# Kernel optimization log

Measured on AMD Instinct MI355X. Metric: run time of the kernel, lower is better.

The kernel has to match this reference:

```python
import jax, jax.numpy as jnp
import numpy as np

B, T, E, H = 8, 2048, 1024, 1024  # batch, seq, embed, head size

def setup_inputs() -> dict:
    key = jax.random.key(0)
    k1, k2, k3, k4 = jax.random.split(key, 4)
    x = jax.random.normal(k1, (B, T, E), dtype=jnp.float32)
    # torch nn.Linear weights are [out, in]; scale down for stability
    Wk = jax.random.normal(k2, (H, E), dtype=jnp.float32) * (E ** -0.5)
    Wq = jax.random.normal(k3, (H, E), dtype=jnp.float32) * (E ** -0.5)
    Wv = jax.random.normal(k4, (H, E), dtype=jnp.float32) * (E ** -0.5)
    return {"x": x, "Wk": Wk, "Wq": Wq, "Wv": Wv}

def reference(x, Wk, Wq, Wv):
    Bx, Tx, Ex = x.shape
    k = jnp.einsum('bte,he->bth', x, Wk)   # [B,T,H]
    q = jnp.einsum('bte,he->bth', x, Wq)
    v = jnp.einsum('bte,he->bth', x, Wv)
    # NOTE: original scales by embed_dim**-0.5 (z = input last dim), not head size
    scores = jnp.einsum('bth,bsh->bts', q, k) * (Ex ** -0.5)  # [B,T,T]
    causal = jnp.tril(jnp.ones((Tx, Tx), dtype=bool))
    scores = jnp.where(causal, scores, -jnp.inf)
    wei = jax.nn.softmax(scores, axis=-1)
    return jnp.einsum('bts,bsh->bth', wei, v)
```

## Files before the change

### kernel.cpp

```cpp
#include <hip/hip_runtime.h>
#include <hip/hip_bf16.h>

typedef unsigned short u16;
typedef __bf16 bf16x8 __attribute__((ext_vector_type(8)));
typedef unsigned short u16x8 __attribute__((ext_vector_type(8)));
typedef unsigned short u16x4 __attribute__((ext_vector_type(4)));
typedef float f32x4 __attribute__((ext_vector_type(4)));
typedef float f32x16 __attribute__((ext_vector_type(16)));

#define B_ 8
#define T_ 2048
#define E_ 1024
#define H_ 1024
#define M_ (B_ * T_)
#define INF __builtin_inff()

__device__ inline u16 f2bf(float f) {
    __bf16 h = (__bf16)f;
    return __builtin_bit_cast(u16, h);
}
__device__ inline float bf2f(u16 u) {
    unsigned v = (unsigned)u << 16;
    return __builtin_bit_cast(float, v);
}
__device__ inline bf16x8 load_frag(const u16* p) {
    u16x8 u = *(const u16x8*)p;
    return __builtin_bit_cast(bf16x8, u);
}
__device__ inline void gload_lds16(const u16* g, u16* l) {
    __builtin_amdgcn_global_load_lds(
        (__attribute__((address_space(1))) unsigned int*)(g),
        (__attribute__((address_space(3))) unsigned int*)(l), 16, 0, 0);
}

__global__ void castk(const float* __restrict__ in, u16* __restrict__ out, int n) {
    int i = (blockIdx.x * blockDim.x + threadIdx.x) * 4;
    if (i < n) {
        f32x4 f = *(const f32x4*)(in + i);
        u16x4 u;
        u[0] = f2bf(f[0]); u[1] = f2bf(f[1]); u[2] = f2bf(f[2]); u[3] = f2bf(f[3]);
        *(u16x4*)(out + i) = u;
    }
}

__global__ __launch_bounds__(512, 1) void gemm_qkv(const u16* __restrict__ A,
                                                   const u16* __restrict__ W,
                                                   u16* __restrict__ qo,
                                                   u16* __restrict__ ko,
                                                   u16* __restrict__ vo) {
    const int id = blockIdx.x;
    const int xcd = id & 7, rr_ = id >> 3;
    const int bm = xcd * 8 + (rr_ & 7);
    const int bn = rr_ >> 3;
    const int tid = threadIdx.x;
    const int w = tid >> 6, lane = tid & 63, quad = lane >> 4, l16 = lane & 15;
    const int wm = w >> 2, wn = w & 3;

    __shared__ u16 smem[65536];

    f32x4 acc[8][4] = {};

    const u16* Ab = A + (size_t)(bm * 256) * E_;
    const u16* Wb = W + (size_t)(bn * 256) * E_;

    auto stage = [&](int buf, int kt) {
        u16* dst = &smem[buf * 16384];
#pragma unroll
        for (int s2 = 0; s2 < 2; s2++) {
            int q = s2 * 512 + tid;
            int row = q >> 2, s = q & 3;
            int c = s ^ (row & 3);
            gload_lds16(Ab + (size_t)row * E_ + kt * 32 + c * 8, &dst[q * 8]);
        }
#pragma unroll
        for (int s2 = 0; s2 < 2; s2++) {
            int q = s2 * 512 + tid;
            int row = q >> 2, s = q & 3;
            int c = s ^ (row & 3);
            gload_lds16(Wb + (size_t)row * E_ + kt * 32 + c * 8, &dst[8192 + q * 8]);
        }
    };

    stage(0, 0); stage(1, 1); stage(2, 2);

    int cur = 0;
    for (int k = 0; k < 32; k++) {
        u16* As = &smem[cur * 16384];
        u16* Bs = As + 8192;

        if (k < 30)      asm volatile("s_waitcnt vmcnt(8)" ::: "memory");
        else if (k == 30) asm volatile("s_waitcnt vmcnt(4)" ::: "memory");
        else              asm volatile("s_waitcnt vmcnt(0)" ::: "memory");
        __builtin_amdgcn_sched_barrier(0);
        __builtin_amdgcn_s_barrier();
        __builtin_amdgcn_sched_barrier(0);

        bf16x8 bfr[4], af[4];
#pragma unroll
        for (int jj = 0; jj < 4; jj++) {
            int R = wn * 64 + jj * 16 + l16;
            bfr[jj] = load_frag(&Bs[(R * 4 + (quad ^ (R & 3))) * 8]);
        }
#pragma unroll
        for (int ii = 0; ii < 4; ii++) {
            int R = wm * 128 + ii * 16 + l16;
            af[ii] = load_frag(&As[(R * 4 + (quad ^ (R & 3))) * 8]);
        }
        asm volatile("s_waitcnt lgkmcnt(0)" ::: "memory");
        __builtin_amdgcn_sched_barrier(0);
        __builtin_amdgcn_s_setprio(1);
#pragma unroll
        for (int ii = 0; ii < 4; ii++)
#pragma unroll
            for (int jj = 0; jj < 4; jj++)
                acc[ii][jj] = __builtin_amdgcn_mfma_f32_16x16x32_bf16(
                    af[ii], bfr[jj], acc[ii][jj], 0, 0, 0);
        __builtin_amdgcn_s_setprio(0);

#pragma unroll
        for (int ii = 0; ii < 4; ii++) {
            int R = wm * 128 + 64 + ii * 16 + l16;
            af[ii] = load_frag(&As[(R * 4 + (quad ^ (R & 3))) * 8]);
        }
        asm volatile("s_waitcnt lgkmcnt(0)" ::: "memory");
        __builtin_amdgcn_sched_barrier(0);
        __builtin_amdgcn_s_setprio(1);
#pragma unroll
        for (int ii = 0; ii < 4; ii++)
#pragma unroll
            for (int jj = 0; jj < 4; jj++)
                acc[4 + ii][jj] = __builtin_amdgcn_mfma_f32_16x16x32_bf16(
                    af[ii], bfr[jj], acc[4 + ii][jj], 0, 0, 0);
        __builtin_amdgcn_s_setprio(0);

        __builtin_amdgcn_s_barrier();
        __builtin_amdgcn_sched_barrier(0);
        if (k + 3 < 32) stage(cur, k + 3);
        cur = (cur == 2) ? 0 : cur + 1;
    }

    if (bn < 8) {
#pragma unroll
        for (int i = 0; i < 8; i++)
#pragma unroll
            for (int j = 0; j < 4; j++) {
                int n = wn * 64 + j * 16 + l16;
#pragma unroll
                for (int rg = 0; rg < 4; rg++) {
                    int m = wm * 128 + i * 16 + quad * 4 + rg;
                    smem[m * 256 + (((n >> 3) ^ (m & 31)) << 3) + (n & 7)] =
                        f2bf(acc[i][j][rg]);
                }
            }
    } else {
#pragma unroll
        for (int i = 0; i < 8; i++)
#pragma unroll
            for (int j = 0; j < 4; j++) {
                int n = wn * 64 + j * 16 + l16;
                int m0 = wm * 128 + i * 16 + quad * 4;
                u16x4 pk;
#pragma unroll
                for (int rg = 0; rg < 4; rg++) pk[rg] = f2bf(acc[i][j][rg]);
                *(u16x4*)&smem[n * 256 + (((m0 >> 3) ^ (n & 31)) << 3) + (m0 & 7)] = pk;
            }
    }
    __syncthreads();

    const int b = bm >> 3;
    if (bn < 4) {
#pragma unroll
        for (int i = 0; i < 16; i++) {
            int c = i * 512 + tid;
            int m = c >> 5, nc = c & 31;
            u16x8 v = *(u16x8*)&smem[m * 256 + ((nc ^ (m & 31)) << 3)];
            *(u16x8*)&qo[(size_t)(bm * 256 + m) * H_ + bn * 256 + nc * 8] = v;
        }
    } else if (bn < 8) {
#pragma unroll
        for (int i = 0; i < 16; i++) {
            int c = i * 512 + tid;
            int ln = c & 63, h16c = (c >> 6) & 15, s32c = c >> 10;
            int m = s32c * 32 + (ln & 31);
            int nc = h16c * 2 + (ln >> 5);
            u16x8 v = *(u16x8*)&smem[m * 256 + ((nc ^ (m & 31)) << 3)];
            int s32g = (bm & 7) * 8 + s32c;
            int h16g = (bn - 4) * 16 + h16c;
            *(u16x8*)&ko[(((size_t)b * 64 + s32g) * 64 + h16g) * 512 + ln * 8] = v;
        }
    } else {
#pragma unroll
        for (int i = 0; i < 16; i++) {
            int c = i * 512 + tid;
            int ln = c & 63, s16c = (c >> 6) & 15, h32c = c >> 10;
            int n = h32c * 32 + (ln & 31);
            int mc = s16c * 2 + (ln >> 5);
            u16x8 v = *(u16x8*)&smem[n * 256 + ((mc ^ (n & 31)) << 3)];
            int h32g = (bn - 8) * 8 + h32c;
            int s16g = (bm & 7) * 16 + s16c;
            *(u16x8*)&vo[(((size_t)b * 32 + h32g) * 128 + s16g) * 512 + ln * 8] = v;
        }
    }
}

__global__ __launch_bounds__(512, 2) void attn(const u16* __restrict__ qb,
                                               const u16* __restrict__ kfg,
                                               const u16* __restrict__ vfg,
                                               float* __restrict__ out) {
    const int bid = blockIdx.x;
    const int b = bid & 7;
    const int qt = bid >> 3;
    const int t0 = (31 - qt) * 64;
    const int tid = threadIdx.x;
    const int w = tid >> 6, lane = tid & 63;
    const int l5 = lane >> 5, l31 = lane & 31;
    const int srow = tid >> 3, sg = tid & 7;

    __shared__ u16 Qs[64 * 1024];
    __shared__ u16 Sp[2 * 64 * 128];
    float* alphas = (float*)(Sp + 8192);

    const u16* qB = qb + (size_t)b * T_ * H_;
    const u16* kfB = kfg + (size_t)b * 2097152;
    const u16* vfB = vfg + (size_t)b * 2097152;
    const float scale = 0.03125f;

#pragma unroll
    for (int i = 0; i < 16; i++) {
        int s = i * 512 + tid;
        int row = s >> 7, c = s & 127;
        int cc = c ^ (row & 7);
        gload_lds16(qB + (size_t)(t0 + row) * H_ + cc * 8, &Qs[s * 8]);
    }

    float m_r = -INF, l_r = 0.f;
    f32x16 o[2][4] = {};

    const int ct = w & 3;
    const int kh = w >> 2;

    __syncthreads();

    for (int s0 = 0; s0 <= t0 + 63; s0 += 128) {
        const u16* vp = vfB + ((size_t)(w * 4) * 128 + (s0 >> 4)) * 512 + lane * 8;
        bf16x8 vbuf[3][4];
#pragma unroll
        for (int ht = 0; ht < 4; ht++)
            vbuf[0][ht] = load_frag(vp + (size_t)ht * 128 * 512);

        f32x16 sa0 = {}, sa1 = {};
        {
            const u16* kp = kfB + (((size_t)((s0 >> 5) + ct)) * 64 + kh * 32) * 512 + lane * 8;
#pragma unroll 8
            for (int st = 0; st < 32; st++) {
                bf16x8 kf = load_frag(kp + st * 512);
                int cb = (kh * 32 + st) * 2 + l5;
                int x0 = l31 & 7;
                bf16x8 a0 = load_frag(&Qs[((size_t)l31 * 128 + (cb ^ x0)) * 8]);
                bf16x8 a1 = load_frag(&Qs[((size_t)(32 + l31) * 128 + (cb ^ x0)) * 8]);
                __builtin_amdgcn_s_setprio(1);
                sa0 = __builtin_amdgcn_mfma_f32_32x32x16_bf16(a0, kf, sa0, 0, 0, 0);
                sa1 = __builtin_amdgcn_mfma_f32_32x32x16_bf16(a1, kf, sa1, 0, 0, 0);
                __builtin_amdgcn_s_setprio(0);
            }
        }
        __syncthreads();
        {
            u16* Sdst = Sp + kh * 8192;
            int col = ct * 32 + l31;
            int chc = col >> 3, cil = col & 7;
#pragma unroll
            for (int reg = 0; reg < 16; reg++) {
                int row = (reg & 3) + 8 * (reg >> 2) + 4 * l5;
                Sdst[(row * 16 + (chc ^ (row & 7))) * 8 + cil] = f2bf(sa0[reg] * scale);
                int row1 = row + 32;
                Sdst[(row1 * 16 + (chc ^ (row1 & 7))) * 8 + cil] = f2bf(sa1[reg] * scale);
            }
        }
        __syncthreads();

        {
            int sw0 = (sg * 2) ^ (srow & 7), sw1 = (sg * 2 + 1) ^ (srow & 7);
            u16x8 a0 = *(u16x8*)&Sp[(srow * 16 + sw0) * 8];
            u16x8 a1 = *(u16x8*)&Sp[(srow * 16 + sw1) * 8];
            u16x8 b0 = *(u16x8*)&Sp[8192 + (srow * 16 + sw0) * 8];
            u16x8 b1 = *(u16x8*)&Sp[8192 + (srow * 16 + sw1) * 8];
            float v[16];
#pragma unroll
            for (int j = 0; j < 8; j++) v[j] = bf2f(a0[j]) + bf2f(b0[j]);
#pragma unroll
            for (int j = 0; j < 8; j++) v[8 + j] = bf2f(a1[j]) + bf2f(b1[j]);
            int colb = sg * 16;
#pragma unroll
            for (int j = 0; j < 16; j++)
                if (s0 + colb + j > t0 + srow) v[j] = -INF;
            float rmax = v[0];
#pragma unroll
            for (int j = 1; j < 16; j++) rmax = fmaxf(rmax, v[j]);
#pragma unroll
            for (int off = 4; off >= 1; off >>= 1) rmax = fmaxf(rmax, __shfl_xor(rmax, off, 64));
            float mn = fmaxf(m_r, rmax);
            float alpha = __expf(m_r - mn);
            float rsum = 0.f;
            u16x8 p0, p1;
#pragma unroll
            for (int j = 0; j < 8; j++) {
                float p = __expf(v[j] - mn);
                rsum += p; p0[j] = f2bf(p);
            }
#pragma unroll
            for (int j = 0; j < 8; j++) {
                float p = __expf(v[8 + j] - mn);
                rsum += p; p1[j] = f2bf(p);
            }
#pragma unroll
            for (int off = 4; off >= 1; off >>= 1) rsum += __shfl_xor(rsum, off, 64);
            l_r = l_r * alpha + rsum;
            m_r = mn;
            *(u16x8*)&Sp[(srow * 16 + sw0) * 8] = p0;
            *(u16x8*)&Sp[(srow * 16 + sw1) * 8] = p1;
            __syncthreads();
            if (sg == 0) alphas[srow] = alpha;
        }
        __syncthreads();

        {
#pragma unroll
            for (int rg = 0; rg < 2; rg++)
#pragma unroll
                for (int reg = 0; reg < 16; reg++) {
                    float al = alphas[rg * 32 + (reg & 3) + 8 * (reg >> 2) + 4 * l5];
#pragma unroll
                    for (int ht = 0; ht < 4; ht++) o[rg][ht][reg] *= al;
                }
            int xp = l31 & 7;
#pragma unroll
            for (int ht = 0; ht < 4; ht++)
                vbuf[1][ht] = load_frag(vp + ((size_t)ht * 128 + 1) * 512);
#pragma unroll
            for (int sc = 0; sc < 8; sc++) {
                if (sc < 6) {
#pragma unroll
                    for (int ht = 0; ht < 4; ht++)
                        vbuf[(sc + 2) % 3][ht] = load_frag(vp + ((size_t)ht * 128 + sc + 2) * 512);
                }
                bf16x8 p0 = load_frag(&Sp[((size_t)l31 * 16 + ((sc * 2 + l5) ^ xp)) * 8]);
                bf16x8 p1 = load_frag(&Sp[((size_t)(32 + l31) * 16 + ((sc * 2 + l5) ^ xp)) * 8]);
                __builtin_amdgcn_s_setprio(1);
#pragma unroll
                for (int ht = 0; ht < 4; ht++) {
                    o[0][ht] = __builtin_amdgcn_mfma_f32_32x32x16_bf16(p0, vbuf[sc % 3][ht], o[0][ht], 0, 0, 0);
                    o[1][ht] = __builtin_amdgcn_mfma_f32_32x32x16_bf16(p1, vbuf[sc % 3][ht], o[1][ht], 0, 0, 0);
                }
                __builtin_amdgcn_s_setprio(0);
            }
        }
    }

    __syncthreads();
    if (sg == 0) alphas[srow] = l_r;
    __syncthreads();
    float* ob = out + (size_t)b * T_ * H_;
#pragma unroll
    for (int rg = 0; rg < 2; rg++)
#pragma unroll
        for (int reg = 0; reg < 16; reg++) {
            int row = rg * 32 + (reg & 3) + 8 * (reg >> 2) + 4 * l5;
            float linv = 1.f / alphas[row];
#pragma unroll
            for (int ht = 0; ht < 4; ht++) {
                int col = w * 128 + ht * 32 + l31;
                ob[(size_t)(t0 + row) * H_ + col] = o[rg][ht][reg] * linv;
            }
        }
}

extern "C" void kernel_launch(void* const* d_in, const int* in_sizes, int n_in,
                              void* d_out, int out_size, void* d_ws, size_t ws_size,
                              hipStream_t stream) {
    const float* x  = (const float*)d_in[0];
    const float* Wk = (const float*)d_in[1];
    const float* Wq = (const float*)d_in[2];
    const float* Wv = (const float*)d_in[3];
    float* out = (float*)d_out;

    char* ws = (char*)d_ws;
    const size_t SZ_XB  = (size_t)M_ * E_ * 2;
    const size_t SZ_W   = (size_t)3 * H_ * E_ * 2;
    const size_t SZ_QKV = (size_t)M_ * H_ * 2;
    u16* xb   = (u16*)(ws);
    u16* wqkv = (u16*)(ws + SZ_XB);
    u16* qb   = (u16*)(ws + SZ_XB + SZ_W);
    u16* kfb  = (u16*)(ws + SZ_XB + SZ_W + SZ_QKV);
    u16* vfb  = (u16*)(ws + SZ_XB + SZ_W + 2 * SZ_QKV);

    castk<<<M_ * E_ / 4 / 256, 256, 0, stream>>>(x, xb, M_ * E_);
    castk<<<H_ * E_ / 4 / 256, 256, 0, stream>>>(Wq, wqkv, H_ * E_);
    castk<<<H_ * E_ / 4 / 256, 256, 0, stream>>>(Wk, wqkv + (size_t)H_ * E_, H_ * E_);
    castk<<<H_ * E_ / 4 / 256, 256, 0, stream>>>(Wv, wqkv + (size_t)2 * H_ * E_, H_ * E_);

    gemm_qkv<<<dim3(768), 512, 0, stream>>>(xb, wqkv, qb, kfb, vfb);

    attn<<<dim3(256), 512, 0, stream>>>(qb, kfb, vfb, out);
}
```

Baseline: 470.3 us.

## Interleave per-matrix global prefetch loads into QKV GEMM MFMA phases

Restructures the QKV projection GEMM pipeline so that the A and W tiles for iteration k+2 are issued separately, each between fragment reads and the MFMA block of one half-iteration. Previously all loads for k+3 were issued together at the end of the iteration with prefetch depth 3. The aim is to spread global-to-LDS traffic across the compute phases. The cost is a shallower prefetch distance and extra workgroup barriers per iteration.

```diff
diff --git a/kernel.cpp b/kernel.cpp
--- a/kernel.cpp
+++ b/kernel.cpp
@@ -63,34 +63,28 @@
     const u16* Ab = A + (size_t)(bm * 256) * E_;
     const u16* Wb = W + (size_t)(bn * 256) * E_;
 
-    auto stage = [&](int buf, int kt) {
-        u16* dst = &smem[buf * 16384];
+    auto stage_mat = [&](int r, int mat, int kt, const u16* gb) {
 #pragma unroll
         for (int s2 = 0; s2 < 2; s2++) {
             int q = s2 * 512 + tid;
             int row = q >> 2, s = q & 3;
             int c = s ^ (row & 3);
-            gload_lds16(Ab + (size_t)row * E_ + kt * 32 + c * 8, &dst[q * 8]);
-        }
-#pragma unroll
-        for (int s2 = 0; s2 < 2; s2++) {
-            int q = s2 * 512 + tid;
-            int row = q >> 2, s = q & 3;
-            int c = s ^ (row & 3);
-            gload_lds16(Wb + (size_t)row * E_ + kt * 32 + c * 8, &dst[8192 + q * 8]);
+            gload_lds16(gb + (size_t)row * E_ + kt * 32 + c * 8,
+                        &smem[r * 16384 + mat * 8192 + (row * 4 + s) * 8]);
         }
     };
 
-    stage(0, 0); stage(1, 1); stage(2, 2);
-
-    int cur = 0;
+    stage_mat(0, 0, 0, Ab); stage_mat(0, 1, 0, Wb);
+    stage_mat(1, 0, 1, Ab); stage_mat(1, 1, 1, Wb);
+
     for (int k = 0; k < 32; k++) {
-        u16* As = &smem[cur * 16384];
+        const int r = k % 3;
+        u16* As = &smem[r * 16384];
         u16* Bs = As + 8192;
-
-        if (k < 30)      asm volatile("s_waitcnt vmcnt(8)" ::: "memory");
-        else if (k == 30) asm volatile("s_waitcnt vmcnt(4)" ::: "memory");
-        else              asm volatile("s_waitcnt vmcnt(0)" ::: "memory");
+        const int r2 = (k + 2) % 3;
+
+        if (k < 31) asm volatile("s_waitcnt vmcnt(4)" ::: "memory");
+        else        asm volatile("s_waitcnt vmcnt(0)" ::: "memory");
         __builtin_amdgcn_sched_barrier(0);
         __builtin_amdgcn_s_barrier();
         __builtin_amdgcn_sched_barrier(0);
@@ -106,6 +100,9 @@
             int R = wm * 128 + ii * 16 + l16;
             af[ii] = load_frag(&As[(R * 4 + (quad ^ (R & 3))) * 8]);
         }
+        if (k + 2 < 32) stage_mat(r2, 0, k + 2, Ab);
+        __builtin_amdgcn_sched_barrier(0);
+        __builtin_amdgcn_s_barrier();
         asm volatile("s_waitcnt lgkmcnt(0)" ::: "memory");
         __builtin_amdgcn_sched_barrier(0);
         __builtin_amdgcn_s_setprio(1);
@@ -116,12 +113,16 @@
                 acc[ii][jj] = __builtin_amdgcn_mfma_f32_16x16x32_bf16(
                     af[ii], bfr[jj], acc[ii][jj], 0, 0, 0);
         __builtin_amdgcn_s_setprio(0);
+        __builtin_amdgcn_s_barrier();
 
 #pragma unroll
         for (int ii = 0; ii < 4; ii++) {
             int R = wm * 128 + 64 + ii * 16 + l16;
             af[ii] = load_frag(&As[(R * 4 + (quad ^ (R & 3))) * 8]);
         }
+        if (k + 2 < 32) stage_mat(r2, 1, k + 2, Wb);
+        __builtin_amdgcn_sched_barrier(0);
+        __builtin_amdgcn_s_barrier();
         asm volatile("s_waitcnt lgkmcnt(0)" ::: "memory");
         __builtin_amdgcn_sched_barrier(0);
         __builtin_amdgcn_s_setprio(1);
@@ -132,11 +133,7 @@
                 acc[4 + ii][jj] = __builtin_amdgcn_mfma_f32_16x16x32_bf16(
                     af[ii], bfr[jj], acc[4 + ii][jj], 0, 0, 0);
         __builtin_amdgcn_s_setprio(0);
-
         __builtin_amdgcn_s_barrier();
-        __builtin_amdgcn_sched_barrier(0);
-        if (k + 3 < 32) stage(cur, k + 3);
-        cur = (cur == 2) ? 0 : cur + 1;
     }
 
     if (bn < 8) {
```

Result: no change. 467.5 us (-0.6%).
